# Kernel tuning notes

Measured on AMD Instinct MI355X. Metric: run time of the kernel, lower is better.

## Reference

```python
import jax, jax.numpy as jnp
from jax import lax
import numpy as np

N_ATOMS = 8192
N_FREE = 4096
ATOM_MASS = 1.0


def setup_inputs() -> dict:
    key = jax.random.key(0)
    k1, k2, k3 = jax.random.split(key, 3)
    q = jax.random.normal(k1, (N_FREE, 3), dtype=jnp.float32)
    qd = jax.random.normal(k2, (N_FREE, 3), dtype=jnp.float32)
    x0 = jax.random.normal(k3, (N_ATOMS, 3), dtype=jnp.float32)
    free_idx = jnp.arange(N_FREE, dtype=jnp.int64 if jax.config.jax_enable_x64 else jnp.int32)
    return {"q": q, "qd": qd, "x0": x0, "free_idx": free_idx}


def reference(q, qd, x0, free_idx):
    # x = x0 with free rows replaced by q; constrained atoms have zero velocity,
    # so T = m/2 * sum(qd^2) exactly (xd is zero elsewhere).
    x = x0.at[free_idx].set(q)
    T = ATOM_MASS / 2 * jnp.sum(qd ** 2)

    # All-pairs potential sum_{i<j} 1/r_ij, then module returns 2*V,
    # i.e. the full sum over ordered pairs i != j of 1/r_ij.
    # Vectorized via ||xi - xj||^2 = |xi|^2 + |xj|^2 - 2 xi.xj (single [N,N] matmul).
    x2 = jnp.sum(x * x, axis=1)                      # [N]
    r2 = x2[:, None] + x2[None, :] - 2.0 * (x @ x.T)  # [N, N]
    n = x.shape[0]
    diag = jnp.eye(n, dtype=bool)
    r2_safe = jnp.where(diag, 1.0, jnp.maximum(r2, 1e-12))
    rinv = jnp.where(diag, 0.0, lax.rsqrt(r2_safe))   # 1/r_ij, zero on diagonal
    V2 = jnp.sum(rinv)                                # == 2 * sum_{i<j} 1/r_ij
    return T - V2
```

## Files before the change

### kernel.cpp

```cpp
#include <hip/hip_runtime.h>

#define NATOMS 8192
#define NFREE  4096

constexpr int TPB = 256;
constexpr int IPT = 2;
constexpr int TI  = TPB * IPT;
constexpr int JT  = 32;
constexpr int GI  = NATOMS / TI;
constexpr int GJ  = NATOMS / JT;
constexpr int TPS = TI / JT;
__device__ __constant__ const int S_START[GI + 1] = {
    0, 256, 496, 720, 928, 1120, 1296, 1456, 1600,
    1728, 1840, 1936, 2016, 2080, 2128, 2160, 2176};
constexpr int NVBLK = 2176;

__device__ __forceinline__ float wave_reduce(float v) {
#pragma unroll
    for (int off = 32; off > 0; off >>= 1)
        v += __shfl_down(v, off, 64);
    return v;
}

__global__ __launch_bounds__(TPB) void pair_kernel(const float* __restrict__ q,
                                                   const float* __restrict__ x0,
                                                   float* __restrict__ vpart) {
    __shared__ float4 sj[JT];
    const int bid = blockIdx.x;

    int x = 0;
#pragma unroll
    for (int e = 1; e < GI; ++e) x += (bid >= S_START[e]);
    const int y  = bid - S_START[x] + TPS * x;
    const int i0 = x * TI;
    const int j0 = y * JT;
    const int t  = threadIdx.x;

    if (t < JT) {
        const int ja = j0 + t;
        const float* src = (ja < NFREE) ? (q + 3 * ja) : (x0 + 3 * (ja - NFREE) + 3 * NFREE);
        const float* p = (ja < NFREE) ? (q + 3 * ja) : (x0 + 3 * ja);
        (void)src;
        float xx = p[0], yy = p[1], zz = p[2];
        sj[t] = make_float4(xx, yy, zz, fmaf(xx, xx, fmaf(yy, yy, zz * zz)));
    }

    float axi[IPT], ayi[IPT], azi[IPT], si[IPT], acc[IPT];
    const float* isrc = (i0 < NFREE) ? q : x0;
#pragma unroll
    for (int k = 0; k < IPT; ++k) {
        const int ia = i0 + t + k * TPB;
        float xx = isrc[3 * ia + 0], yy = isrc[3 * ia + 1], zz = isrc[3 * ia + 2];
        axi[k] = -2.f * xx;
        ayi[k] = -2.f * yy;
        azi[k] = -2.f * zz;
        si[k]  = fmaf(xx, xx, fmaf(yy, yy, zz * zz));
        acc[k] = 0.f;
    }
    __syncthreads();

    const int rel0 = j0 - i0;
    if (rel0 < TI) {
        int m[IPT];
#pragma unroll
        for (int k = 0; k < IPT; ++k) m[k] = t + k * TPB - rel0;
#pragma unroll 8
        for (int j = 0; j < JT; ++j) {
            const float4 pj = sj[j];
#pragma unroll
            for (int k = 0; k < IPT; ++k) {
                float d = fmaf(axi[k], pj.x, si[k]);
                d = fmaf(ayi[k], pj.y, d);
                d = fmaf(azi[k], pj.z, d);
                float rinv = __builtin_amdgcn_rsqf(d + pj.w);
                acc[k] += (m[k] < j) ? rinv : 0.f;
            }
        }
    } else {
#pragma unroll 8
        for (int j = 0; j < JT; ++j) {
            const float4 pj = sj[j];
#pragma unroll
            for (int k = 0; k < IPT; ++k) {
                float d = fmaf(axi[k], pj.x, si[k]);
                d = fmaf(ayi[k], pj.y, d);
                d = fmaf(azi[k], pj.z, d);
                acc[k] += __builtin_amdgcn_rsqf(d + pj.w);
            }
        }
    }

    float v = acc[0] + acc[1];
    v = wave_reduce(v);
    __shared__ float s[TPB / 64];
    int lane = t & 63, wid = t >> 6;
    if (lane == 0) s[wid] = v;
    __syncthreads();
    if (t == 0)
        vpart[bid] = (s[0] + s[1]) + (s[2] + s[3]);
}

__global__ void finalize(const float* __restrict__ vpart,
                         const float4* __restrict__ qd4,
                         float* __restrict__ out) {
    float v = 0.f;
    for (int i = threadIdx.x; i < NVBLK; i += TPB) v += vpart[i];
    float tq = 0.f;
    for (int i = threadIdx.x; i < (NFREE * 3) / 4; i += TPB) {
        float4 u = qd4[i];
        tq += fmaf(u.x, u.x, fmaf(u.y, u.y, fmaf(u.z, u.z, u.w * u.w)));
    }
    v = wave_reduce(v);
    tq = wave_reduce(tq);
    __shared__ float sv[TPB / 64], st[TPB / 64];
    int lane = threadIdx.x & 63, wid = threadIdx.x >> 6;
    if (lane == 0) { sv[wid] = v; st[wid] = tq; }
    __syncthreads();
    if (threadIdx.x == 0) {
        float V = (sv[0] + sv[1]) + (sv[2] + sv[3]);
        float T = (st[0] + st[1]) + (st[2] + st[3]);
        out[0] = 0.5f * T - 2.0f * V;
    }
}

extern "C" void kernel_launch(void* const* d_in, const int* in_sizes, int n_in,
                              void* d_out, int out_size, void* d_ws, size_t ws_size,
                              hipStream_t stream) {
    const float* q        = (const float*)d_in[0];
    const float* qd       = (const float*)d_in[1];
    const float* x0       = (const float*)d_in[2];
    float* out = (float*)d_out;

    float* vpart = (float*)d_ws;

    pair_kernel<<<NVBLK, TPB, 0, stream>>>(q, x0, vpart);
    finalize<<<1, TPB, 0, stream>>>(vpart, (const float4*)qd, out);
}
```

Before: 18.98 us.

## Use packed FP32 FMA for pair distances and double rows per thread

Each thread now handles four i-atoms instead of two, and the distance computation for pairs of i-atoms uses v_pk_fma_f32/v_pk_add_f32 inline asm with op_sel broadcasting. The triangular block schedule table is regenerated for the larger i-tile, which roughly halves the block count. The aim is to cut VALU instruction count per pair and amortize the shared j-tile loads over more rows. The trade-off is fewer blocks and more registers per thread, which may lower occupancy and tail balance on a 256-CU device.

```diff
diff --git a/kernel.cpp b/kernel.cpp
--- a/kernel.cpp
+++ b/kernel.cpp
@@ -4,16 +4,35 @@
 #define NFREE  4096
 
 constexpr int TPB = 256;
-constexpr int IPT = 2;
+constexpr int IPT = 4;
 constexpr int TI  = TPB * IPT;
 constexpr int JT  = 32;
 constexpr int GI  = NATOMS / TI;
 constexpr int GJ  = NATOMS / JT;
 constexpr int TPS = TI / JT;
-__device__ __constant__ const int S_START[GI + 1] = {
-    0, 256, 496, 720, 928, 1120, 1296, 1456, 1600,
-    1728, 1840, 1936, 2016, 2080, 2128, 2160, 2176};
-constexpr int NVBLK = 2176;
+__device__ __constant__ const int S_START[GI + 1] = {0, 256, 480, 672, 832, 960, 1056, 1120, 1152};
+constexpr int NVBLK = 1152;
+
+typedef __attribute__((ext_vector_type(2))) float f32x2;
+
+__device__ __forceinline__ f32x2 pk_fma_blo(f32x2 a, f32x2 b, f32x2 c) {
+    f32x2 d;
+    asm("v_pk_fma_f32 %0, %1, %2, %3 op_sel:[0,0,0] op_sel_hi:[1,0,1]"
+        : "=v"(d) : "v"(a), "v"(b), "v"(c));
+    return d;
+}
+__device__ __forceinline__ f32x2 pk_fma_bhi(f32x2 a, f32x2 b, f32x2 c) {
+    f32x2 d;
+    asm("v_pk_fma_f32 %0, %1, %2, %3 op_sel:[0,1,0] op_sel_hi:[1,1,1]"
+        : "=v"(d) : "v"(a), "v"(b), "v"(c));
+    return d;
+}
+__device__ __forceinline__ f32x2 pk_add_bhi(f32x2 a, f32x2 b) {
+    f32x2 d;
+    asm("v_pk_add_f32 %0, %1, %2 op_sel:[0,1] op_sel_hi:[1,1]"
+        : "=v"(d) : "v"(a), "v"(b));
+    return d;
+}
 
 __device__ __forceinline__ float wave_reduce(float v) {
 #pragma unroll
@@ -38,59 +57,66 @@
 
     if (t < JT) {
         const int ja = j0 + t;
-        const float* src = (ja < NFREE) ? (q + 3 * ja) : (x0 + 3 * (ja - NFREE) + 3 * NFREE);
         const float* p = (ja < NFREE) ? (q + 3 * ja) : (x0 + 3 * ja);
-        (void)src;
         float xx = p[0], yy = p[1], zz = p[2];
         sj[t] = make_float4(xx, yy, zz, fmaf(xx, xx, fmaf(yy, yy, zz * zz)));
     }
 
-    float axi[IPT], ayi[IPT], azi[IPT], si[IPT], acc[IPT];
     const float* isrc = (i0 < NFREE) ? q : x0;
+    f32x2 ax2[IPT / 2], ay2[IPT / 2], az2[IPT / 2], s2[IPT / 2];
+    float acc[IPT];
+    int m[IPT];
+    const int rel0 = j0 - i0;
 #pragma unroll
     for (int k = 0; k < IPT; ++k) {
         const int ia = i0 + t + k * TPB;
         float xx = isrc[3 * ia + 0], yy = isrc[3 * ia + 1], zz = isrc[3 * ia + 2];
-        axi[k] = -2.f * xx;
-        ayi[k] = -2.f * yy;
-        azi[k] = -2.f * zz;
-        si[k]  = fmaf(xx, xx, fmaf(yy, yy, zz * zz));
+        ax2[k / 2][k & 1] = -2.f * xx;
+        ay2[k / 2][k & 1] = -2.f * yy;
+        az2[k / 2][k & 1] = -2.f * zz;
+        s2[k / 2][k & 1]  = fmaf(xx, xx, fmaf(yy, yy, zz * zz));
         acc[k] = 0.f;
+        m[k] = t + k * TPB - rel0;
     }
     __syncthreads();
 
-    const int rel0 = j0 - i0;
     if (rel0 < TI) {
-        int m[IPT];
-#pragma unroll
-        for (int k = 0; k < IPT; ++k) m[k] = t + k * TPB - rel0;
 #pragma unroll 8
         for (int j = 0; j < JT; ++j) {
             const float4 pj = sj[j];
+            f32x2 pxy; pxy.x = pj.x; pxy.y = pj.y;
+            f32x2 pzw; pzw.x = pj.z; pzw.y = pj.w;
 #pragma unroll
-            for (int k = 0; k < IPT; ++k) {
-                float d = fmaf(axi[k], pj.x, si[k]);
-                d = fmaf(ayi[k], pj.y, d);
-                d = fmaf(azi[k], pj.z, d);
-                float rinv = __builtin_amdgcn_rsqf(d + pj.w);
-                acc[k] += (m[k] < j) ? rinv : 0.f;
+            for (int g = 0; g < IPT / 2; ++g) {
+                f32x2 d = pk_fma_blo(ax2[g], pxy, s2[g]);
+                d = pk_fma_bhi(ay2[g], pxy, d);
+                d = pk_fma_blo(az2[g], pzw, d);
+                d = pk_add_bhi(d, pzw);
+                float r0 = __builtin_amdgcn_rsqf(d.x);
+                float r1 = __builtin_amdgcn_rsqf(d.y);
+                acc[2 * g + 0] += (m[2 * g + 0] < j) ? r0 : 0.f;
+                acc[2 * g + 1] += (m[2 * g + 1] < j) ? r1 : 0.f;
             }
         }
     } else {
 #pragma unroll 8
         for (int j = 0; j < JT; ++j) {
             const float4 pj = sj[j];
+            f32x2 pxy; pxy.x = pj.x; pxy.y = pj.y;
+            f32x2 pzw; pzw.x = pj.z; pzw.y = pj.w;
 #pragma unroll
-            for (int k = 0; k < IPT; ++k) {
-                float d = fmaf(axi[k], pj.x, si[k]);
-                d = fmaf(ayi[k], pj.y, d);
-                d = fmaf(azi[k], pj.z, d);
-                acc[k] += __builtin_amdgcn_rsqf(d + pj.w);
+            for (int g = 0; g < IPT / 2; ++g) {
+                f32x2 d = pk_fma_blo(ax2[g], pxy, s2[g]);
+                d = pk_fma_bhi(ay2[g], pxy, d);
+                d = pk_fma_blo(az2[g], pzw, d);
+                d = pk_add_bhi(d, pzw);
+                acc[2 * g + 0] += __builtin_amdgcn_rsqf(d.x);
+                acc[2 * g + 1] += __builtin_amdgcn_rsqf(d.y);
             }
         }
     }
 
-    float v = acc[0] + acc[1];
+    float v = (acc[0] + acc[1]) + (acc[2] + acc[3]);
     v = wave_reduce(v);
     __shared__ float s[TPB / 64];
     int lane = t & 63, wid = t >> 6;
@@ -126,9 +152,9 @@
 extern "C" void kernel_launch(void* const* d_in, const int* in_sizes, int n_in,
                               void* d_out, int out_size, void* d_ws, size_t ws_size,
                               hipStream_t stream) {
-    const float* q        = (const float*)d_in[0];
-    const float* qd       = (const float*)d_in[1];
-    const float* x0       = (const float*)d_in[2];
+    const float* q  = (const float*)d_in[0];
+    const float* qd = (const float*)d_in[1];
+    const float* x0 = (const float*)d_in[2];
     float* out = (float*)d_out;
 
     float* vpart = (float*)d_ws;
```

Result: faster. 17.30 us (-8.8%).

## Load j-tile into registers via uniform loads and widen i-tile per thread

Applied to the files above, without the earlier changes.

Drops the shared-memory j-tile and its barrier: each thread reads the block-uniform j coordinates straight from global memory into registers, which the compiler can turn into scalar loads. Each thread now handles 4 i atoms instead of 2 and the j tile shrinks to 16, with the triangular block schedule table recomputed to match. The aim is to remove LDS traffic and sync overhead and raise reuse per loaded j value. The trade-offs are higher register pressure and more total blocks, plus the fully unrolled j loop.

```diff
diff --git a/kernel.cpp b/kernel.cpp
--- a/kernel.cpp
+++ b/kernel.cpp
@@ -4,16 +4,15 @@
 #define NFREE  4096
 
 constexpr int TPB = 256;
-constexpr int IPT = 2;
+constexpr int IPT = 4;
 constexpr int TI  = TPB * IPT;
-constexpr int JT  = 32;
+constexpr int JT  = 16;
 constexpr int GI  = NATOMS / TI;
 constexpr int GJ  = NATOMS / JT;
 constexpr int TPS = TI / JT;
 __device__ __constant__ const int S_START[GI + 1] = {
-    0, 256, 496, 720, 928, 1120, 1296, 1456, 1600,
-    1728, 1840, 1936, 2016, 2080, 2128, 2160, 2176};
-constexpr int NVBLK = 2176;
+    0, 512, 960, 1344, 1664, 1920, 2112, 2240, 2304};
+constexpr int NVBLK = 2304;
 
 __device__ __forceinline__ float wave_reduce(float v) {
 #pragma unroll
@@ -25,7 +24,6 @@
 __global__ __launch_bounds__(TPB) void pair_kernel(const float* __restrict__ q,
                                                    const float* __restrict__ x0,
                                                    float* __restrict__ vpart) {
-    __shared__ float4 sj[JT];
     const int bid = blockIdx.x;
 
     int x = 0;
@@ -36,17 +34,10 @@
     const int j0 = y * JT;
     const int t  = threadIdx.x;
 
-    if (t < JT) {
-        const int ja = j0 + t;
-        const float* src = (ja < NFREE) ? (q + 3 * ja) : (x0 + 3 * (ja - NFREE) + 3 * NFREE);
-        const float* p = (ja < NFREE) ? (q + 3 * ja) : (x0 + 3 * ja);
-        (void)src;
-        float xx = p[0], yy = p[1], zz = p[2];
-        sj[t] = make_float4(xx, yy, zz, fmaf(xx, xx, fmaf(yy, yy, zz * zz)));
-    }
-
+    const float* isrc = (i0 < NFREE) ? q : x0;
     float axi[IPT], ayi[IPT], azi[IPT], si[IPT], acc[IPT];
-    const float* isrc = (i0 < NFREE) ? q : x0;
+    int m[IPT];
+    const int rel0 = j0 - i0;
 #pragma unroll
     for (int k = 0; k < IPT; ++k) {
         const int ia = i0 + t + k * TPB;
@@ -56,41 +47,45 @@
         azi[k] = -2.f * zz;
         si[k]  = fmaf(xx, xx, fmaf(yy, yy, zz * zz));
         acc[k] = 0.f;
+        m[k] = t + k * TPB - rel0;
     }
-    __syncthreads();
 
-    const int rel0 = j0 - i0;
+    const float* jp = ((j0 < NFREE) ? q : x0) + 3 * j0;
+    float jx[JT], jy[JT], jz[JT], jw[JT];
+#pragma unroll
+    for (int jj = 0; jj < JT; ++jj) {
+        jx[jj] = jp[3 * jj + 0];
+        jy[jj] = jp[3 * jj + 1];
+        jz[jj] = jp[3 * jj + 2];
+        jw[jj] = fmaf(jx[jj], jx[jj], fmaf(jy[jj], jy[jj], jz[jj] * jz[jj]));
+    }
+
     if (rel0 < TI) {
-        int m[IPT];
 #pragma unroll
-        for (int k = 0; k < IPT; ++k) m[k] = t + k * TPB - rel0;
-#pragma unroll 8
         for (int j = 0; j < JT; ++j) {
-            const float4 pj = sj[j];
 #pragma unroll
             for (int k = 0; k < IPT; ++k) {
-                float d = fmaf(axi[k], pj.x, si[k]);
-                d = fmaf(ayi[k], pj.y, d);
-                d = fmaf(azi[k], pj.z, d);
-                float rinv = __builtin_amdgcn_rsqf(d + pj.w);
+                float d = fmaf(axi[k], jx[j], si[k]);
+                d = fmaf(ayi[k], jy[j], d);
+                d = fmaf(azi[k], jz[j], d);
+                float rinv = __builtin_amdgcn_rsqf(d + jw[j]);
                 acc[k] += (m[k] < j) ? rinv : 0.f;
             }
         }
     } else {
-#pragma unroll 8
+#pragma unroll
         for (int j = 0; j < JT; ++j) {
-            const float4 pj = sj[j];
 #pragma unroll
             for (int k = 0; k < IPT; ++k) {
-                float d = fmaf(axi[k], pj.x, si[k]);
-                d = fmaf(ayi[k], pj.y, d);
-                d = fmaf(azi[k], pj.z, d);
-                acc[k] += __builtin_amdgcn_rsqf(d + pj.w);
+                float d = fmaf(axi[k], jx[j], si[k]);
+                d = fmaf(ayi[k], jy[j], d);
+                d = fmaf(azi[k], jz[j], d);
+                acc[k] += __builtin_amdgcn_rsqf(d + jw[j]);
             }
         }
     }
 
-    float v = acc[0] + acc[1];
+    float v = (acc[0] + acc[1]) + (acc[2] + acc[3]);
     v = wave_reduce(v);
     __shared__ float s[TPB / 64];
     int lane = t & 63, wid = t >> 6;
@@ -104,15 +99,15 @@
                          const float4* __restrict__ qd4,
                          float* __restrict__ out) {
     float v = 0.f;
-    for (int i = threadIdx.x; i < NVBLK; i += TPB) v += vpart[i];
+    for (int i = threadIdx.x; i < NVBLK; i += 256) v += vpart[i];
     float tq = 0.f;
-    for (int i = threadIdx.x; i < (NFREE * 3) / 4; i += TPB) {
+    for (int i = threadIdx.x; i < (NFREE * 3) / 4; i += 256) {
         float4 u = qd4[i];
         tq += fmaf(u.x, u.x, fmaf(u.y, u.y, fmaf(u.z, u.z, u.w * u.w)));
     }
     v = wave_reduce(v);
     tq = wave_reduce(tq);
-    __shared__ float sv[TPB / 64], st[TPB / 64];
+    __shared__ float sv[4], st[4];
     int lane = threadIdx.x & 63, wid = threadIdx.x >> 6;
     if (lane == 0) { sv[wid] = v; st[wid] = tq; }
     __syncthreads();
@@ -126,13 +121,13 @@
 extern "C" void kernel_launch(void* const* d_in, const int* in_sizes, int n_in,
                               void* d_out, int out_size, void* d_ws, size_t ws_size,
                               hipStream_t stream) {
-    const float* q        = (const float*)d_in[0];
-    const float* qd       = (const float*)d_in[1];
-    const float* x0       = (const float*)d_in[2];
+    const float* q  = (const float*)d_in[0];
+    const float* qd = (const float*)d_in[1];
+    const float* x0 = (const float*)d_in[2];
     float* out = (float*)d_out;
 
     float* vpart = (float*)d_ws;
 
     pair_kernel<<<NVBLK, TPB, 0, stream>>>(q, x0, vpart);
-    finalize<<<1, TPB, 0, stream>>>(vpart, (const float4*)qd, out);
+    finalize<<<1, 256, 0, stream>>>(vpart, (const float4*)qd, out);
 }
```

After: 18.91 us. No clear change (-0.4%).
